# Kernel optimization log

Measured on AMD Instinct MI355X. Metric: run time of the kernel, lower is better.

The kernel has to match this reference:

```python
import jax, jax.numpy as jnp
import numpy as np

B, S, D, R, H, NC, NE = 4, 2048, 1024, 512, 8, 8, 8
DH = R // H


def setup_inputs() -> dict:
    key = jax.random.key(0)
    ks = jax.random.split(key, 8)
    x = jax.random.normal(ks[0], (B, S, D), dtype=jnp.float32)
    # causal mask [B,1,S,S]: True where attention allowed
    mask = jnp.broadcast_to(jnp.tril(jnp.ones((S, S), dtype=bool)), (B, 1, S, S))
    compress_neurons = jax.random.normal(ks[1], (NC, D, R), dtype=jnp.float32) / np.sqrt(D)
    expand_neurons = jax.random.normal(ks[2], (NE, R, D), dtype=jnp.float32) / np.sqrt(R)
    w_router_q = jax.random.normal(ks[3], (NC, D), dtype=jnp.float32) / np.sqrt(D)
    w_router_k = jax.random.normal(ks[4], (NC, D), dtype=jnp.float32) / np.sqrt(D)
    w_router_v = jax.random.normal(ks[5], (NC, D), dtype=jnp.float32) / np.sqrt(D)
    w_router_o = jax.random.normal(ks[6], (NE, R), dtype=jnp.float32) / np.sqrt(R)
    return {"x": x, "mask": mask, "compress_neurons": compress_neurons,
            "expand_neurons": expand_neurons, "w_router_q": w_router_q,
            "w_router_k": w_router_k, "w_router_v": w_router_v,
            "w_router_o": w_router_o}


def _compress(x, w_router, neurons):
    # x: [B,S,D], w_router: [N,D], neurons: [N,D,R] -> [B,S,R]
    weights = jax.nn.softmax(jnp.einsum('bsd,nd->bsn', x, w_router), axis=-1)
    all_proj = jnp.einsum('bsd,ndr->bsnr', x, neurons)
    return jnp.einsum('bsnr,bsn->bsr', all_proj, weights)


def _expand(x, w_router, neurons):
    # x: [B,S,R], w_router: [N,R], neurons: [N,R,D] -> [B,S,D]
    weights = jax.nn.softmax(jnp.einsum('bsr,nr->bsn', x, w_router), axis=-1)
    all_proj = jnp.einsum('bsr,nrd->bsnd', x, neurons)
    return jnp.einsum('bsnd,bsn->bsd', all_proj, weights)


def reference(x, mask, compress_neurons, expand_neurons,
              w_router_q, w_router_k, w_router_v, w_router_o):
    q = _compress(x, w_router_q, compress_neurons)  # [B,S,R]
    k = _compress(x, w_router_k, compress_neurons)
    v = _compress(x, w_router_v, compress_neurons)
    # [B,H,S,DH]
    q = q.reshape(B, S, H, DH).transpose(0, 2, 1, 3)
    k = k.reshape(B, S, H, DH).transpose(0, 2, 1, 3)
    v = v.reshape(B, S, H, DH).transpose(0, 2, 1, 3)
    scores = jnp.einsum('bhqd,bhkd->bhqk', q, k) / jnp.sqrt(jnp.float32(DH))
    scores = jnp.where(mask, scores, jnp.float32(-jnp.inf))
    attn = jax.nn.softmax(scores, axis=-1)
    attn_out = jnp.einsum('bhqk,bhkd->bhqd', attn, v)
    attn_out = attn_out.transpose(0, 2, 1, 3).reshape(B, S, R)
    return _expand(attn_out, w_router_o, expand_neurons)
```

## Files before the change

### kernel.cpp

```cpp
#include <hip/hip_runtime.h>
#include <hip/hip_bf16.h>

typedef unsigned short u16;
typedef __attribute__((ext_vector_type(8))) short s8v;
typedef __attribute__((ext_vector_type(4))) float f4v;

#define Bb 4
#define Ss 2048
#define Dd 1024
#define Rr 512
#define Hh 8
#define DHd 64
#define Mm 8192

__device__ __forceinline__ float bf2f(u16 u){
    union { unsigned int i; float f; } v; v.i = ((unsigned int)u)<<16; return v.f;
}
__device__ __forceinline__ u16 f2bf(float f){
    __hip_bfloat16 h = __float2bfloat16(f);
    return *(u16*)&h;
}
__device__ __forceinline__ void gld_lds16(const u16* g, u16* l){
    __builtin_amdgcn_global_load_lds((const __attribute__((address_space(1))) unsigned int*)g,
                                     (__attribute__((address_space(3))) unsigned int*)l, 16, 0, 0);
}

__global__ __launch_bounds__(256) void k_f2b(
    const float* __restrict__ in, u16* __restrict__ out)
{
    const size_t i = (size_t)blockIdx.x*256 + threadIdx.x;
    float4 v = ((const float4*)in)[i];
    ushort4 o;
    o.x = f2bf(v.x); o.y = f2bf(v.y); o.z = f2bf(v.z); o.w = f2bf(v.w);
    ((ushort4*)out)[i] = o;
}

__global__ __launch_bounds__(256) void k_transpose_f2b(
    const float* __restrict__ src, u16* __restrict__ dst, int A, int B)
{
    __shared__ float t[64][65];
    const int a0 = blockIdx.x*64, b0 = blockIdx.y*64, n = blockIdx.z;
    const size_t sbase = (size_t)n*A*B;
    const int r = threadIdx.x>>4, c = threadIdx.x&15;
#pragma unroll
    for (int p=0;p<4;p++){
        const int ar = r + p*16;
        float4 v = *(const float4*)(src + sbase + (size_t)(a0+ar)*B + b0 + c*4);
        t[ar][c*4+0]=v.x; t[ar][c*4+1]=v.y; t[ar][c*4+2]=v.z; t[ar][c*4+3]=v.w;
    }
    __syncthreads();
#pragma unroll
    for (int p=0;p<4;p++){
        const int br = r + p*16;
        ushort4 o;
        o.x = f2bf(t[c*4+0][br]); o.y = f2bf(t[c*4+1][br]);
        o.z = f2bf(t[c*4+2][br]); o.w = f2bf(t[c*4+3][br]);
        *(ushort4*)(dst + sbase + (size_t)(b0+br)*A + a0 + c*4) = o;
    }
}

__global__ __launch_bounds__(256) void k_transpose_v(
    const u16* __restrict__ vb, u16* __restrict__ vtb)
{
    __shared__ u16 T[64][72];
    const int st = blockIdx.x, bh = blockIdx.y;
    const int b = bh>>3, h = bh&7;
    const int tid = threadIdx.x;
    const int srow = tid>>2, c4 = tid&3;
#pragma unroll
    for (int p=0;p<2;p++){
        const int ch = c4 + p*4;
        s8v v = *(const s8v*)(vb + (size_t)(b*Ss + st*64 + srow)*Rr + h*DHd + ch*8);
        *(s8v*)&T[srow][ch*8] = v;
    }
    __syncthreads();
    const int dl = tid & 63, w2 = tid>>6;
#pragma unroll
    for (int p=0;p<2;p++){
        const int sc = w2*2 + p;
        u16 o[8];
#pragma unroll
        for (int j=0;j<8;j++) o[j] = T[sc*8+j][dl];
        *(s8v*)(vtb + (size_t)bh*DHd*Ss + (size_t)dl*Ss + st*64 + sc*8) = *(s8v*)o;
    }
}

__global__ __launch_bounds__(64) void k_router_qkv(
    const float* __restrict__ x, const float* __restrict__ wrq,
    const float* __restrict__ wrk, const float* __restrict__ wrv,
    float* __restrict__ wq, float* __restrict__ wk, float* __restrict__ wv)
{
    const int m = blockIdx.x, lane = threadIdx.x;
    float aq[8], ak[8], av[8];
#pragma unroll
    for (int r=0;r<8;r++){ aq[r]=0.f; ak[r]=0.f; av[r]=0.f; }
#pragma unroll
    for (int i=0;i<4;i++){
        const size_t d0 = i*256 + lane*4;
        float4 xv = *(const float4*)(x + (size_t)m*Dd + d0);
#pragma unroll
        for (int r=0;r<8;r++){
            float4 q4 = *(const float4*)(wrq + (size_t)r*Dd + d0);
            aq[r] += xv.x*q4.x + xv.y*q4.y + xv.z*q4.z + xv.w*q4.w;
            float4 k4 = *(const float4*)(wrk + (size_t)r*Dd + d0);
            ak[r] += xv.x*k4.x + xv.y*k4.y + xv.z*k4.z + xv.w*k4.w;
            float4 v4 = *(const float4*)(wrv + (size_t)r*Dd + d0);
            av[r] += xv.x*v4.x + xv.y*v4.y + xv.z*v4.z + xv.w*v4.w;
        }
    }
#pragma unroll
    for (int r=0;r<8;r++){
#pragma unroll
        for (int off=32;off>=1;off>>=1){
            aq[r]+=__shfl_xor(aq[r],off);
            ak[r]+=__shfl_xor(ak[r],off);
            av[r]+=__shfl_xor(av[r],off);
        }
    }
    float mq=aq[0], mk=ak[0], mv=av[0];
#pragma unroll
    for (int r=1;r<8;r++){ mq=fmaxf(mq,aq[r]); mk=fmaxf(mk,ak[r]); mv=fmaxf(mv,av[r]); }
    float eq[8], ek[8], ev[8], sq=0.f, sk=0.f, sv=0.f;
#pragma unroll
    for (int r=0;r<8;r++){
        eq[r]=expf(aq[r]-mq); sq+=eq[r];
        ek[r]=expf(ak[r]-mk); sk+=ek[r];
        ev[r]=expf(av[r]-mv); sv+=ev[r];
    }
    if (lane < 8)        wq[m*8+lane]    = eq[lane]/sq;
    else if (lane < 16)  wk[m*8+lane-8]  = ek[lane-8]/sk;
    else if (lane < 24)  wv[m*8+lane-16] = ev[lane-16]/sv;
}

__global__ __launch_bounds__(256) void k_compress_mfma(
    const u16* __restrict__ xb, const u16* __restrict__ cnT,
    const float* __restrict__ wq, const float* __restrict__ wk, const float* __restrict__ wv,
    u16* __restrict__ qb, u16* __restrict__ kb, u16* __restrict__ vb)
{
    __shared__ __align__(16) u16 As[128*64];
    __shared__ __align__(16) u16 Bs[64*64];
    __shared__ float wL[3][8][128];
    const int tid = threadIdx.x;
    const int lane = tid & 63, w = tid >> 6;
    const int quad = lane >> 4, l15 = lane & 15;
    const int m0 = blockIdx.x*128, r0 = blockIdx.y*64;
    for (int i = tid; i < 3*8*128; i += 256){
        const int t = i >> 10, rem = i & 1023, n = rem >> 7, ml = rem & 127;
        const float* wsrc = (t==0)? wq : (t==1)? wk : wv;
        wL[t][n][ml] = wsrc[(size_t)(m0+ml)*8 + n];
    }
    const int wm = (w&1)*64, wr = (w>>1)*32;
    const int srow = lane>>3;
    const int sch  = (lane&7) ^ srow;
    f4v accq[4][2], acck[4][2], accv[4][2];
    const f4v fz = {0.f,0.f,0.f,0.f};
#pragma unroll
    for (int mt=0;mt<4;mt++)
#pragma unroll
        for (int rt=0;rt<2;rt++){ accq[mt][rt]=fz; acck[mt][rt]=fz; accv[mt][rt]=fz; }
    for (int n=0;n<8;n++){
        f4v cacc[4][2];
#pragma unroll
        for (int mt=0;mt<4;mt++)
#pragma unroll
            for (int rt=0;rt<2;rt++) cacc[mt][rt]=fz;
        const size_t bbase = (size_t)(n*512 + r0)*1024;
        for (int s=0;s<16;s++){
            const int d0 = s*64;
            __syncthreads();
#pragma unroll
            for (int i=0;i<4;i++)
                gld_lds16(xb + (size_t)(m0 + i*32 + w*8 + srow)*Dd + d0 + sch*8,
                          As + (i*32 + w*8)*64);
#pragma unroll
            for (int i=0;i<2;i++)
                gld_lds16(cnT + bbase + (size_t)(i*32 + w*8 + srow)*1024 + d0 + sch*8,
                          Bs + (i*32 + w*8)*64);
            __syncthreads();
            s8v af[4][2], bf[2][2];
#pragma unroll
            for (int mt=0;mt<4;mt++)
#pragma unroll
                for (int kc=0;kc<2;kc++)
                    af[mt][kc] = *(const s8v*)(As + (wm + mt*16 + l15)*64 + (((kc*4+quad) ^ (l15&7))<<3));
#pragma unroll
            for (int rt=0;rt<2;rt++)
#pragma unroll
                for (int kc=0;kc<2;kc++)
                    bf[rt][kc] = *(const s8v*)(Bs + (wr + rt*16 + l15)*64 + (((kc*4+quad) ^ (l15&7))<<3));
#pragma unroll
            for (int mt=0;mt<4;mt++)
#pragma unroll
                for (int rt=0;rt<2;rt++){
                    cacc[mt][rt] = __builtin_amdgcn_mfma_f32_16x16x32_bf16(af[mt][0], bf[rt][0], cacc[mt][rt], 0,0,0);
                    cacc[mt][rt] = __builtin_amdgcn_mfma_f32_16x16x32_bf16(af[mt][1], bf[rt][1], cacc[mt][rt], 0,0,0);
                }
        }
#pragma unroll
        for (int mt=0;mt<4;mt++){
            const int mq4 = wm + mt*16 + (quad<<2);
            f4v w0 = *(const f4v*)&wL[0][n][mq4];
            f4v w1 = *(const f4v*)&wL[1][n][mq4];
            f4v w2 = *(const f4v*)&wL[2][n][mq4];
#pragma unroll
            for (int rt=0;rt<2;rt++){
                accq[mt][rt] += w0 * cacc[mt][rt];
                acck[mt][rt] += w1 * cacc[mt][rt];
                accv[mt][rt] += w2 * cacc[mt][rt];
            }
        }
    }
#pragma unroll
    for (int mt=0;mt<4;mt++)
#pragma unroll
        for (int rt=0;rt<2;rt++){
            const int rcol = r0 + wr + rt*16 + l15;
#pragma unroll
            for (int e=0;e<4;e++){
                const int m = m0 + wm + mt*16 + (quad<<2) + e;
                const size_t idx = (size_t)m*Rr + rcol;
                qb[idx] = f2bf(accq[mt][rt][e]);
                kb[idx] = f2bf(acck[mt][rt][e]);
                vb[idx] = f2bf(accv[mt][rt][e]);
            }
        }
}

__global__ __launch_bounds__(256) void k_attn_mfma(
    const u16* __restrict__ qb, const u16* __restrict__ kb, const u16* __restrict__ vtb,
    u16* __restrict__ ab)
{
    __shared__ __align__(16) u16 Ks[64*64];
    __shared__ __align__(16) u16 Vt[64*64];
    __shared__ __align__(16) u16 Ps[4*16*64];
    const int tid = threadIdx.x;
    const int lane = tid & 63, w = tid >> 6;
    const int quad = lane >> 4, l15 = lane & 15;
    const int bh = blockIdx.x;
    const int yq = blockIdx.y;
    const int qt = (yq < 16) ? yq : (47 - yq);
    const int b = bh >> 3, h = bh & 7;
    const u16* qbase = qb + (size_t)(b*Ss)*Rr + h*DHd;
    const u16* kbase = kb + (size_t)(b*Ss)*Rr + h*DHd;
    const u16* vtbase = vtb + (size_t)bh*DHd*Ss;
    s8v qf[2];
    {
        const size_t qrow = qt*64 + w*16 + l15;
        qf[0] = *(const s8v*)(qbase + qrow*Rr + quad*8);
        qf[1] = *(const s8v*)(qbase + qrow*Rr + 32 + quad*8);
    }
    const f4v fz = {0.f,0.f,0.f,0.f};
    f4v oacc[4];
#pragma unroll
    for (int dn=0;dn<4;dn++) oacc[dn]=fz;
    float m_e[4], l_e[4];
#pragma unroll
    for (int e=0;e<4;e++){ m_e[e] = -1e30f; l_e[e] = 0.f; }
    const int srow = lane>>3;
    const int sch  = (lane&7) ^ srow;
    u16* pw = Ps + w*1024;
    for (int kt=0; kt<=qt; kt++){
        __syncthreads();
        gld_lds16(kbase + (size_t)(kt*64 + w*8 + srow)*Rr + sch*8,        Ks + w*512);
        gld_lds16(kbase + (size_t)(kt*64 + 32 + w*8 + srow)*Rr + sch*8,   Ks + 2048 + w*512);
        gld_lds16(vtbase + (size_t)(w*8 + srow)*Ss + kt*64 + sch*8,       Vt + w*512);
        gld_lds16(vtbase + (size_t)(32 + w*8 + srow)*Ss + kt*64 + sch*8,  Vt + 2048 + w*512);
        __syncthreads();
        f4v s[4];
#pragma unroll
        for (int cn=0;cn<4;cn++) s[cn]=fz;
#pragma unroll
        for (int cn=0;cn<4;cn++)
#pragma unroll
            for (int kc=0;kc<2;kc++){
                s8v bf = *(const s8v*)(Ks + (cn*16 + l15)*64 + (((kc*4 + quad) ^ (l15&7))<<3));
                s[cn] = __builtin_amdgcn_mfma_f32_16x16x32_bf16(qf[kc], bf, s[cn], 0,0,0);
            }
        if (kt == qt){
            const int qg = qt*64 + w*16 + quad*4;
            const int kg = kt*64 + l15;
#pragma unroll
            for (int cn=0;cn<4;cn++)
#pragma unroll
                for (int e=0;e<4;e++){
                    float sv = s[cn][e]*0.125f;
                    s[cn][e] = ((kg + cn*16) > (qg + e)) ? -1e30f : sv;
                }
        } else {
#pragma unroll
            for (int cn=0;cn<4;cn++)
#pragma unroll
                for (int e=0;e<4;e++) s[cn][e] *= 0.125f;
        }
        float al_e[4];
#pragma unroll
        for (int e=0;e<4;e++){
            float mx = fmaxf(fmaxf(s[0][e],s[1][e]), fmaxf(s[2][e],s[3][e]));
#pragma unroll
            for (int off=1;off<16;off<<=1) mx = fmaxf(mx, __shfl_xor(mx, off));
            const float mt = fmaxf(m_e[e], mx);
            const float al = __expf(m_e[e] - mt);
            m_e[e] = mt;
            float sum = 0.f;
#pragma unroll
            for (int cn=0;cn<4;cn++){
                float p = __expf(s[cn][e] - mt);
                s[cn][e] = p; sum += p;
            }
#pragma unroll
            for (int off=1;off<16;off<<=1) sum += __shfl_xor(sum, off);
            l_e[e] = l_e[e]*al + sum;
            al_e[e] = al;
        }
#pragma unroll
        for (int e=0;e<4;e++){
            const int row = quad*4 + e;
#pragma unroll
            for (int cn=0;cn<4;cn++){
                const int key = cn*16 + l15;
                pw[row*64 + (((key>>3) ^ (row&7))<<3) + (key&7)] = f2bf(s[cn][e]);
            }
        }
#pragma unroll
        for (int dn=0;dn<4;dn++)
#pragma unroll
            for (int e=0;e<4;e++) oacc[dn][e] *= al_e[e];
#pragma unroll
        for (int dn=0;dn<4;dn++)
#pragma unroll
            for (int kc=0;kc<2;kc++){
                s8v pf = *(const s8v*)(pw + l15*64 + (((kc*4 + quad) ^ (l15&7))<<3));
                s8v vf = *(const s8v*)(Vt + (dn*16 + l15)*64 + (((kc*4 + quad) ^ (l15&7))<<3));
                oacc[dn] = __builtin_amdgcn_mfma_f32_16x16x32_bf16(pf, vf, oacc[dn], 0,0,0);
            }
    }
    u16* abase = ab + (size_t)(b*Ss + qt*64 + w*16)*Rr + h*DHd;
#pragma unroll
    for (int e=0;e<4;e++){
        const float inv = 1.f / l_e[e];
#pragma unroll
        for (int dn=0;dn<4;dn++)
            abase[(size_t)(quad*4+e)*Rr + dn*16 + l15] = f2bf(oacc[dn][e]*inv);
    }
}

__global__ __launch_bounds__(64) void k_router_o(
    const u16* __restrict__ ab, const float* __restrict__ wro, float* __restrict__ wo)
{
    const int m = blockIdx.x, lane = threadIdx.x;
    float a[8];
#pragma unroll
    for (int r=0;r<8;r++) a[r]=0.f;
#pragma unroll
    for (int i=0;i<2;i++){
        const size_t d0 = i*256 + lane*4;
        ushort4 av4 = *(const ushort4*)(ab + (size_t)m*Rr + d0);
        float a0=bf2f(av4.x), a1=bf2f(av4.y), a2=bf2f(av4.z), a3=bf2f(av4.w);
#pragma unroll
        for (int r=0;r<8;r++){
            float4 w4 = *(const float4*)(wro + (size_t)r*Rr + d0);
            a[r] += a0*w4.x + a1*w4.y + a2*w4.z + a3*w4.w;
        }
    }
#pragma unroll
    for (int r=0;r<8;r++)
#pragma unroll
        for (int off=32;off>=1;off>>=1) a[r]+=__shfl_xor(a[r],off);
    float mx=a[0];
#pragma unroll
    for (int r=1;r<8;r++) mx=fmaxf(mx,a[r]);
    float e[8], s=0.f;
#pragma unroll
    for (int r=0;r<8;r++){ e[r]=expf(a[r]-mx); s+=e[r]; }
    if (lane < 8) wo[m*8+lane] = e[lane]/s;
}

__global__ __launch_bounds__(256) void k_expand_mfma(
    const u16* __restrict__ ab, const u16* __restrict__ enT,
    const float* __restrict__ wo, float* __restrict__ out)
{
    __shared__ __align__(16) u16 As[128*64];
    __shared__ __align__(16) u16 Bs[64*64];
    __shared__ float wL[8][128];
    const int tid = threadIdx.x;
    const int lane = tid & 63, w = tid >> 6;
    const int quad = lane >> 4, l15 = lane & 15;
    const int m0 = blockIdx.x*128, dB0 = blockIdx.y*64;
    for (int i = tid; i < 8*128; i += 256){
        const int n = i >> 7, ml = i & 127;
        wL[n][ml] = wo[(size_t)(m0+ml)*8 + n];
    }
    const int wm = (w&1)*64, wr = (w>>1)*32;
    const int srow = lane>>3;
    const int sch  = (lane&7) ^ srow;
    f4v acc[4][2];
    const f4v fz = {0.f,0.f,0.f,0.f};
#pragma unroll
    for (int mt=0;mt<4;mt++)
#pragma unroll
        for (int rt=0;rt<2;rt++) acc[mt][rt]=fz;
    for (int n=0;n<8;n++){
        f4v cacc[4][2];
#pragma unroll
        for (int mt=0;mt<4;mt++)
#pragma unroll
            for (int rt=0;rt<2;rt++) cacc[mt][rt]=fz;
        const size_t bbase = (size_t)(n*1024 + dB0)*512;
        for (int s=0;s<8;s++){
            const int r0k = s*64;
            __syncthreads();
#pragma unroll
            for (int i=0;i<4;i++)
                gld_lds16(ab + (size_t)(m0 + i*32 + w*8 + srow)*Rr + r0k + sch*8,
                          As + (i*32 + w*8)*64);
#pragma unroll
            for (int i=0;i<2;i++)
                gld_lds16(enT + bbase + (size_t)(i*32 + w*8 + srow)*512 + r0k + sch*8,
                          Bs + (i*32 + w*8)*64);
            __syncthreads();
            s8v af[4][2], bf[2][2];
#pragma unroll
            for (int mt=0;mt<4;mt++)
#pragma unroll
                for (int kc=0;kc<2;kc++)
                    af[mt][kc] = *(const s8v*)(As + (wm + mt*16 + l15)*64 + (((kc*4+quad) ^ (l15&7))<<3));
#pragma unroll
            for (int rt=0;rt<2;rt++)
#pragma unroll
                for (int kc=0;kc<2;kc++)
                    bf[rt][kc] = *(const s8v*)(Bs + (wr + rt*16 + l15)*64 + (((kc*4+quad) ^ (l15&7))<<3));
#pragma unroll
            for (int mt=0;mt<4;mt++)
#pragma unroll
                for (int rt=0;rt<2;rt++){
                    cacc[mt][rt] = __builtin_amdgcn_mfma_f32_16x16x32_bf16(af[mt][0], bf[rt][0], cacc[mt][rt], 0,0,0);
                    cacc[mt][rt] = __builtin_amdgcn_mfma_f32_16x16x32_bf16(af[mt][1], bf[rt][1], cacc[mt][rt], 0,0,0);
                }
        }
#pragma unroll
        for (int mt=0;mt<4;mt++){
            const int mq4 = wm + mt*16 + (quad<<2);
            f4v w0 = *(const f4v*)&wL[n][mq4];
#pragma unroll
            for (int rt=0;rt<2;rt++) acc[mt][rt] += w0 * cacc[mt][rt];
        }
    }
#pragma unroll
    for (int mt=0;mt<4;mt++)
#pragma unroll
        for (int rt=0;rt<2;rt++){
            const int dcol = dB0 + wr + rt*16 + l15;
#pragma unroll
            for (int e=0;e<4;e++){
                const int m = m0 + wm + mt*16 + (quad<<2) + e;
                out[(size_t)m*Dd + dcol] = acc[mt][rt][e];
            }
        }
}

extern "C" void kernel_launch(void* const* d_in, const int* in_sizes, int n_in,
                              void* d_out, int out_size, void* d_ws, size_t ws_size,
                              hipStream_t stream) {
    (void)in_sizes; (void)n_in; (void)out_size; (void)ws_size;
    const float* x   = (const float*)d_in[0];
    const float* cn  = (const float*)d_in[2];
    const float* en  = (const float*)d_in[3];
    const float* wrq = (const float*)d_in[4];
    const float* wrk = (const float*)d_in[5];
    const float* wrv = (const float*)d_in[6];
    const float* wro = (const float*)d_in[7];

    float* ws = (float*)d_ws;
    float* wq = ws;
    float* wk = wq + Mm*8;
    float* wv = wk + Mm*8;
    float* wo = wv + Mm*8;
    u16* xb  = (u16*)(wo + Mm*8);
    u16* qb  = xb + (size_t)Mm*Dd;
    u16* kb  = qb + (size_t)Mm*Rr;
    u16* vb  = kb + (size_t)Mm*Rr;
    u16* ab  = vb + (size_t)Mm*Rr;
    u16* cnT = ab + (size_t)Mm*Rr;
    u16* enT = cnT + (size_t)8*Rr*Dd;
    u16* vtb = enT + (size_t)8*Dd*Rr;

    k_f2b<<<Mm*Dd/1024, 256, 0, stream>>>(x, xb);
    k_transpose_f2b<<<dim3(Dd/64, Rr/64, 8), 256, 0, stream>>>(cn, cnT, Dd, Rr);
    k_transpose_f2b<<<dim3(Rr/64, Dd/64, 8), 256, 0, stream>>>(en, enT, Rr, Dd);
    k_router_qkv<<<Mm, 64, 0, stream>>>(x, wrq, wrk, wrv, wq, wk, wv);
    k_compress_mfma<<<dim3(Mm/128, Rr/64), 256, 0, stream>>>(xb, cnT, wq, wk, wv, qb, kb, vb);
    k_transpose_v<<<dim3(Ss/64, Bb*Hh), 256, 0, stream>>>(vb, vtb);
    k_attn_mfma<<<dim3(Bb*Hh, Ss/64), 256, 0, stream>>>(qb, kb, vtb, ab);
    k_router_o<<<Mm, 64, 0, stream>>>(ab, wro, wo);
    k_expand_mfma<<<dim3(Mm/128, Dd/64), 256, 0, stream>>>(ab, enT, wo, (float*)d_out);
}
```

Before: 459.5 us.

## Double-buffer LDS tiles in compress and expand GEMM kernels

Gives the compress and expand MFMA kernels two LDS buffers each, and flattens the neuron and k-step loops into one pipelined loop. The next tile's global-to-LDS loads are issued before computing on the current tile, with one barrier per iteration instead of two. The per-neuron routing-weight accumulation moves into the flattened loop on the last step of each neuron. This roughly doubles LDS use per block, which can reduce occupancy. The overlap only helps if the compiler does not insert a full vmcnt wait before the LDS reads.

```diff
diff --git a/kernel.cpp b/kernel.cpp
--- a/kernel.cpp
+++ b/kernel.cpp
@@ -137,8 +137,8 @@
     const float* __restrict__ wq, const float* __restrict__ wk, const float* __restrict__ wv,
     u16* __restrict__ qb, u16* __restrict__ kb, u16* __restrict__ vb)
 {
-    __shared__ __align__(16) u16 As[128*64];
-    __shared__ __align__(16) u16 Bs[64*64];
+    __shared__ __align__(16) u16 As[2][128*64];
+    __shared__ __align__(16) u16 Bs[2][64*64];
     __shared__ float wL[3][8][128];
     const int tid = threadIdx.x;
     const int lane = tid & 63, w = tid >> 6;
@@ -152,61 +152,66 @@
     const int wm = (w&1)*64, wr = (w>>1)*32;
     const int srow = lane>>3;
     const int sch  = (lane&7) ^ srow;
-    f4v accq[4][2], acck[4][2], accv[4][2];
+    auto stage = [&](int t){
+        const int bi = t & 1;
+        const int n = t >> 4, s = t & 15;
+        const int d0 = s*64;
+        const size_t bbase = (size_t)(n*512 + r0)*1024;
+        u16* Ad = As[bi]; u16* Bd = Bs[bi];
+#pragma unroll
+        for (int i=0;i<4;i++)
+            gld_lds16(xb + (size_t)(m0 + i*32 + w*8 + srow)*Dd + d0 + sch*8,
+                      Ad + (i*32 + w*8)*64);
+#pragma unroll
+        for (int i=0;i<2;i++)
+            gld_lds16(cnT + bbase + (size_t)(i*32 + w*8 + srow)*1024 + d0 + sch*8,
+                      Bd + (i*32 + w*8)*64);
+    };
+    f4v accq[4][2], acck[4][2], accv[4][2], cacc[4][2];
     const f4v fz = {0.f,0.f,0.f,0.f};
 #pragma unroll
     for (int mt=0;mt<4;mt++)
 #pragma unroll
-        for (int rt=0;rt<2;rt++){ accq[mt][rt]=fz; acck[mt][rt]=fz; accv[mt][rt]=fz; }
-    for (int n=0;n<8;n++){
-        f4v cacc[4][2];
+        for (int rt=0;rt<2;rt++){ accq[mt][rt]=fz; acck[mt][rt]=fz; accv[mt][rt]=fz; cacc[mt][rt]=fz; }
+    stage(0);
+    for (int t=0; t<128; t++){
+        __syncthreads();
+        if (t+1 < 128) stage(t+1);
+        const int bi = t & 1;
+        const u16* Ac = As[bi]; const u16* Bc = Bs[bi];
+        s8v af[4][2], bf[2][2];
 #pragma unroll
         for (int mt=0;mt<4;mt++)
 #pragma unroll
-            for (int rt=0;rt<2;rt++) cacc[mt][rt]=fz;
-        const size_t bbase = (size_t)(n*512 + r0)*1024;
-        for (int s=0;s<16;s++){
-            const int d0 = s*64;
-            __syncthreads();
-#pragma unroll
-            for (int i=0;i<4;i++)
-                gld_lds16(xb + (size_t)(m0 + i*32 + w*8 + srow)*Dd + d0 + sch*8,
-                          As + (i*32 + w*8)*64);
-#pragma unroll
-            for (int i=0;i<2;i++)
-                gld_lds16(cnT + bbase + (size_t)(i*32 + w*8 + srow)*1024 + d0 + sch*8,
-                          Bs + (i*32 + w*8)*64);
-            __syncthreads();
-            s8v af[4][2], bf[2][2];
-#pragma unroll
-            for (int mt=0;mt<4;mt++)
-#pragma unroll
-                for (int kc=0;kc<2;kc++)
-                    af[mt][kc] = *(const s8v*)(As + (wm + mt*16 + l15)*64 + (((kc*4+quad) ^ (l15&7))<<3));
-#pragma unroll
-            for (int rt=0;rt<2;rt++)
-#pragma unroll
-                for (int kc=0;kc<2;kc++)
-                    bf[rt][kc] = *(const s8v*)(Bs + (wr + rt*16 + l15)*64 + (((kc*4+quad) ^ (l15&7))<<3));
-#pragma unroll
-            for (int mt=0;mt<4;mt++)
+            for (int kc=0;kc<2;kc++)
+                af[mt][kc] = *(const s8v*)(Ac + (wm + mt*16 + l15)*64 + (((kc*4+quad) ^ (l15&7))<<3));
+#pragma unroll
+        for (int rt=0;rt<2;rt++)
+#pragma unroll
+            for (int kc=0;kc<2;kc++)
+                bf[rt][kc] = *(const s8v*)(Bc + (wr + rt*16 + l15)*64 + (((kc*4+quad) ^ (l15&7))<<3));
+#pragma unroll
+        for (int mt=0;mt<4;mt++)
+#pragma unroll
+            for (int rt=0;rt<2;rt++){
+                cacc[mt][rt] = __builtin_amdgcn_mfma_f32_16x16x32_bf16(af[mt][0], bf[rt][0], cacc[mt][rt], 0,0,0);
+                cacc[mt][rt] = __builtin_amdgcn_mfma_f32_16x16x32_bf16(af[mt][1], bf[rt][1], cacc[mt][rt], 0,0,0);
+            }
+        if ((t & 15) == 15){
+            const int n = t >> 4;
+#pragma unroll
+            for (int mt=0;mt<4;mt++){
+                const int mq4 = wm + mt*16 + (quad<<2);
+                f4v w0 = *(const f4v*)&wL[0][n][mq4];
+                f4v w1 = *(const f4v*)&wL[1][n][mq4];
+                f4v w2 = *(const f4v*)&wL[2][n][mq4];
 #pragma unroll
                 for (int rt=0;rt<2;rt++){
-                    cacc[mt][rt] = __builtin_amdgcn_mfma_f32_16x16x32_bf16(af[mt][0], bf[rt][0], cacc[mt][rt], 0,0,0);
-                    cacc[mt][rt] = __builtin_amdgcn_mfma_f32_16x16x32_bf16(af[mt][1], bf[rt][1], cacc[mt][rt], 0,0,0);
+                    accq[mt][rt] += w0 * cacc[mt][rt];
+                    acck[mt][rt] += w1 * cacc[mt][rt];
+                    accv[mt][rt] += w2 * cacc[mt][rt];
+                    cacc[mt][rt] = fz;
                 }
-        }
-#pragma unroll
-        for (int mt=0;mt<4;mt++){
-            const int mq4 = wm + mt*16 + (quad<<2);
-            f4v w0 = *(const f4v*)&wL[0][n][mq4];
-            f4v w1 = *(const f4v*)&wL[1][n][mq4];
-            f4v w2 = *(const f4v*)&wL[2][n][mq4];
-#pragma unroll
-            for (int rt=0;rt<2;rt++){
-                accq[mt][rt] += w0 * cacc[mt][rt];
-                acck[mt][rt] += w1 * cacc[mt][rt];
-                accv[mt][rt] += w2 * cacc[mt][rt];
             }
         }
     }
@@ -379,8 +384,8 @@
     const u16* __restrict__ ab, const u16* __restrict__ enT,
     const float* __restrict__ wo, float* __restrict__ out)
 {
-    __shared__ __align__(16) u16 As[128*64];
-    __shared__ __align__(16) u16 Bs[64*64];
+    __shared__ __align__(16) u16 As[2][128*64];
+    __shared__ __align__(16) u16 Bs[2][64*64];
     __shared__ float wL[8][128];
     const int tid = threadIdx.x;
     const int lane = tid & 63, w = tid >> 6;
@@ -393,56 +398,63 @@
     const int wm = (w&1)*64, wr = (w>>1)*32;
     const int srow = lane>>3;
     const int sch  = (lane&7) ^ srow;
-    f4v acc[4][2];
+    auto stage = [&](int t){
+        const int bi = t & 1;
+        const int n = t >> 3, s = t & 7;
+        const int r0k = s*64;
+        const size_t bbase = (size_t)(n*1024 + dB0)*512;
+        u16* Ad = As[bi]; u16* Bd = Bs[bi];
+#pragma unroll
+        for (int i=0;i<4;i++)
+            gld_lds16(ab + (size_t)(m0 + i*32 + w*8 + srow)*Rr + r0k + sch*8,
+                      Ad + (i*32 + w*8)*64);
+#pragma unroll
+        for (int i=0;i<2;i++)
+            gld_lds16(enT + bbase + (size_t)(i*32 + w*8 + srow)*512 + r0k + sch*8,
+                      Bd + (i*32 + w*8)*64);
+    };
+    f4v acc[4][2], cacc[4][2];
     const f4v fz = {0.f,0.f,0.f,0.f};
 #pragma unroll
     for (int mt=0;mt<4;mt++)
 #pragma unroll
-        for (int rt=0;rt<2;rt++) acc[mt][rt]=fz;
-    for (int n=0;n<8;n++){
-        f4v cacc[4][2];
+        for (int rt=0;rt<2;rt++){ acc[mt][rt]=fz; cacc[mt][rt]=fz; }
+    stage(0);
+    for (int t=0; t<64; t++){
+        __syncthreads();
+        if (t+1 < 64) stage(t+1);
+        const int bi = t & 1;
+        const u16* Ac = As[bi]; const u16* Bc = Bs[bi];
+        s8v af[4][2], bf[2][2];
 #pragma unroll
         for (int mt=0;mt<4;mt++)
 #pragma unroll
-            for (int rt=0;rt<2;rt++) cacc[mt][rt]=fz;
-        const size_t bbase = (size_t)(n*1024 + dB0)*512;
-        for (int s=0;s<8;s++){
-            const int r0k = s*64;
-            __syncthreads();
-#pragma unroll
-            for (int i=0;i<4;i++)
-                gld_lds16(ab + (size_t)(m0 + i*32 + w*8 + srow)*Rr + r0k + sch*8,
-                          As + (i*32 + w*8)*64);
-#pragma unroll
-            for (int i=0;i<2;i++)
-                gld_lds16(enT + bbase + (size_t)(i*32 + w*8 + srow)*512 + r0k + sch*8,
-                          Bs + (i*32 + w*8)*64);
-            __syncthreads();
-            s8v af[4][2], bf[2][2];
-#pragma unroll
-            for (int mt=0;mt<4;mt++)
-#pragma unroll
-                for (int kc=0;kc<2;kc++)
-                    af[mt][kc] = *(const s8v*)(As + (wm + mt*16 + l15)*64 + (((kc*4+quad) ^ (l15&7))<<3));
-#pragma unroll
-            for (int rt=0;rt<2;rt++)
-#pragma unroll
-                for (int kc=0;kc<2;kc++)
-                    bf[rt][kc] = *(const s8v*)(Bs + (wr + rt*16 + l15)*64 + (((kc*4+quad) ^ (l15&7))<<3));
-#pragma unroll
-            for (int mt=0;mt<4;mt++)
+            for (int kc=0;kc<2;kc++)
+                af[mt][kc] = *(const s8v*)(Ac + (wm + mt*16 + l15)*64 + (((kc*4+quad) ^ (l15&7))<<3));
+#pragma unroll
+        for (int rt=0;rt<2;rt++)
+#pragma unroll
+            for (int kc=0;kc<2;kc++)
+                bf[rt][kc] = *(const s8v*)(Bc + (wr + rt*16 + l15)*64 + (((kc*4+quad) ^ (l15&7))<<3));
+#pragma unroll
+        for (int mt=0;mt<4;mt++)
+#pragma unroll
+            for (int rt=0;rt<2;rt++){
+                cacc[mt][rt] = __builtin_amdgcn_mfma_f32_16x16x32_bf16(af[mt][0], bf[rt][0], cacc[mt][rt], 0,0,0);
+                cacc[mt][rt] = __builtin_amdgcn_mfma_f32_16x16x32_bf16(af[mt][1], bf[rt][1], cacc[mt][rt], 0,0,0);
+            }
+        if ((t & 7) == 7){
+            const int n = t >> 3;
+#pragma unroll
+            for (int mt=0;mt<4;mt++){
+                const int mq4 = wm + mt*16 + (quad<<2);
+                f4v w0 = *(const f4v*)&wL[n][mq4];
 #pragma unroll
                 for (int rt=0;rt<2;rt++){
-                    cacc[mt][rt] = __builtin_amdgcn_mfma_f32_16x16x32_bf16(af[mt][0], bf[rt][0], cacc[mt][rt], 0,0,0);
-                    cacc[mt][rt] = __builtin_amdgcn_mfma_f32_16x16x32_bf16(af[mt][1], bf[rt][1], cacc[mt][rt], 0,0,0);
+                    acc[mt][rt] += w0 * cacc[mt][rt];
+                    cacc[mt][rt] = fz;
                 }
-        }
-#pragma unroll
-        for (int mt=0;mt<4;mt++){
-            const int mq4 = wm + mt*16 + (quad<<2);
-            f4v w0 = *(const f4v*)&wL[n][mq4];
-#pragma unroll
-            for (int rt=0;rt<2;rt++) acc[mt][rt] += w0 * cacc[mt][rt];
+            }
         }
     }
 #pragma unroll
```

After: 477.5 us. +3.9%, slower.
